# Kernel optimization log

Hardware: AMD Instinct MI355X
Metric: run time of the kernel (lower is better)

The kernel has to match this reference:

```python
import jax, jax.numpy as jnp
import numpy as np

LOG2E = 1.4426950408889634
NUM_HEADS = 12

def fake_quant_sym8(x):
    # per-tensor symmetric int8 fake-quant (QuantStub with MovingAverageMinMax,
    # symmetric, qint8 [-128,127]); dynamic scale from current amax, STE.
    scale = jnp.maximum(jnp.max(jnp.abs(x)) / 127.0, 1e-8)
    q = jnp.clip(jnp.round(x / scale), -128.0, 127.0) * scale
    return x + jax.lax.stop_gradient(q - x)

def integer_approx_softmax(x):
    # ITA-style integer-approximated softmax: exp(x) = 2^(x*log2e),
    # split into integer/fractional parts, 2^f approximated piecewise-linearly
    # as (1 + f) for f in [0,1) (hardware shift-add friendly), then normalize.
    z = x * LOG2E
    z = z - jnp.max(z, axis=-1, keepdims=True)  # z <= 0, numerically stable
    zi = jnp.floor(z)
    zf = z - zi
    p = jnp.exp2(zi) * (1.0 + zf)
    return p / jnp.sum(p, axis=-1, keepdims=True)

def setup_inputs() -> dict:
    key = jax.random.key(0)
    ks = jax.random.split(key, 5)
    B, N, E, P = 8, 1024, 768, 768
    s = 0.02  # typical init scale for linear weights
    return {
        "x":  jax.random.normal(ks[0], (B, N, E), jnp.float32),
        "Wq": jax.random.normal(ks[1], (E, P), jnp.float32) * s,
        "bq": jnp.zeros((P,), jnp.float32),
        "Wk": jax.random.normal(ks[2], (E, P), jnp.float32) * s,
        "bk": jnp.zeros((P,), jnp.float32),
        "Wv": jax.random.normal(ks[3], (E, P), jnp.float32) * s,
        "bv": jnp.zeros((P,), jnp.float32),
        "Wo": jax.random.normal(ks[4], (P, E), jnp.float32) * s,
        "bo": jnp.zeros((E,), jnp.float32),
    }

def reference(x, Wq, bq, Wk, bk, Wv, bv, Wo, bo):
    B, N, E = x.shape
    H = NUM_HEADS
    D = Wq.shape[1] // H  # head_dim = proj_dim // num_heads
    xq = fake_quant_sym8(x)
    # projections -> [B, H, N, D]
    Q = (xq @ Wq + bq).reshape(B, N, H, D).transpose(0, 2, 1, 3)
    K = (xq @ Wk + bk).reshape(B, N, H, D).transpose(0, 2, 1, 3)
    V = (xq @ Wv + bv).reshape(B, N, H, D).transpose(0, 2, 1, 3)
    # NOTE: no 1/sqrt(D) scaling -- the torch module applies none (ITA absorbs
    # scaling into the quantization parameters).
    logits = jnp.einsum('bhnd,bhmd->bhnm', Q, K)
    attn = integer_approx_softmax(logits)
    ctx = jnp.einsum('bhnm,bhmd->bhnd', attn, V)
    ctx = ctx.transpose(0, 2, 1, 3).reshape(B, N, H * D)
    return ctx @ Wo + bo
```

## Files before the change

### kernel.cpp

```cpp
#include <hip/hip_runtime.h>


typedef unsigned short u16;
typedef __attribute__((ext_vector_type(8))) short short8;
typedef __attribute__((ext_vector_type(8))) _Float16 half8;
typedef __attribute__((ext_vector_type(4))) float f32x4;

#define LOG2E_F 1.4426950408889634f

static __device__ __forceinline__ half8 s2h(short8 s) {
  union { short8 s; half8 h; } u; u.s = s; return u.h;
}
static __device__ __forceinline__ f32x4 mfma16(short8 a, short8 b, f32x4 c) {
  return __builtin_amdgcn_mfma_f32_16x16x32_f16(s2h(a), s2h(b), c, 0, 0, 0);
}
static __device__ __forceinline__ u16 f2h(float f) {
  union { _Float16 h; u16 u; } v; v.h = (_Float16)f; return v.u;
}
static __device__ __forceinline__ void gload16(const void* g, void* l) {
  __builtin_amdgcn_global_load_lds(
      (const __attribute__((address_space(1))) void*)g,
      (__attribute__((address_space(3))) void*)l, 16, 0, 0);
}

__global__ __launch_bounds__(256) void amax_part_kernel(
    const float4* __restrict__ x, float* __restrict__ part, int n4) {
  float m = 0.f;
  int i = blockIdx.x * 256 + threadIdx.x;
  const int stride = gridDim.x * 256;
  for (; i < n4; i += stride) {
    float4 v = x[i];
    m = fmaxf(m, fmaxf(fmaxf(fabsf(v.x), fabsf(v.y)),
                       fmaxf(fabsf(v.z), fabsf(v.w))));
  }
  #pragma unroll
  for (int o = 1; o < 64; o <<= 1) m = fmaxf(m, __shfl_xor(m, o));
  __shared__ float sw[4];
  if ((threadIdx.x & 63) == 0) sw[threadIdx.x >> 6] = m;
  __syncthreads();
  if (threadIdx.x == 0)
    part[blockIdx.x] = fmaxf(fmaxf(sw[0], sw[1]), fmaxf(sw[2], sw[3]));
}

__global__ __launch_bounds__(256) void amax_fin_kernel(
    const float* __restrict__ part, double* __restrict__ dsc,
    float* __restrict__ dscf) {
  const int t = threadIdx.x;
  float m = fmaxf(fmaxf(part[t], part[t + 256]),
                  fmaxf(part[t + 512], part[t + 768]));
  #pragma unroll
  for (int o = 1; o < 64; o <<= 1) m = fmaxf(m, __shfl_xor(m, o));
  __shared__ float sw[4];
  if ((t & 63) == 0) sw[t >> 6] = m;
  __syncthreads();
  if (t == 0) {
    double sd = (double)(fmaxf(fmaxf(sw[0], sw[1]), fmaxf(sw[2], sw[3]))) / 127.0;
    if (sd < 1e-8) sd = 1e-8;
    dsc[0] = sd;
    dsc[1] = 1.0 / sd;
    dscf[0] = (float)sd;
  }
}

__global__ __launch_bounds__(256) void quant_kernel(
    const float4* __restrict__ x, u16* __restrict__ xq,
    const double* __restrict__ dsc, int n4) {
  const double rinv = dsc[1];
  int i = blockIdx.x * 256 + threadIdx.x;
  const int stride = gridDim.x * 256;
  for (; i < n4; i += stride) {
    float4 v = x[i];
    ushort4 u;
    u.x = f2h((float)fmin(fmax(rint((double)v.x * rinv), -128.0), 127.0));
    u.y = f2h((float)fmin(fmax(rint((double)v.y * rinv), -128.0), 127.0));
    u.z = f2h((float)fmin(fmax(rint((double)v.z * rinv), -128.0), 127.0));
    u.w = f2h((float)fmin(fmax(rint((double)v.w * rinv), -128.0), 127.0));
    *(ushort4*)&xq[(size_t)i * 4] = u;
  }
}

__global__ __launch_bounds__(256) void prep_weights_kernel(
    const float* __restrict__ Wq, const float* __restrict__ Wk,
    const float* __restrict__ Wv, const float* __restrict__ Wo,
    const float* __restrict__ bq, const float* __restrict__ bk,
    const float* __restrict__ bv,
    u16* __restrict__ Wcat, u16* __restrict__ Wot, float* __restrict__ bcat) {
  __shared__ float t[64][65];
  const int m = blockIdx.y;
  const float* src = (m == 0) ? Wq : (m == 1) ? Wk : (m == 2) ? Wv : Wo;
  u16* dst = (m == 3) ? Wot : (Wcat + (size_t)m * 768 * 768);
  const int tile = blockIdx.x;
  const int r0 = (tile / 12) * 64, c0 = (tile - (tile / 12) * 12) * 64;
  const int i = threadIdx.x >> 6, j = threadIdx.x & 63;
  #pragma unroll
  for (int it = 0; it < 16; ++it) {
    const int row = it * 4 + i;
    t[row][j] = src[(size_t)(r0 + row) * 768 + c0 + j];
  }
  __syncthreads();
  #pragma unroll
  for (int it = 0; it < 16; ++it) {
    const int row = it * 4 + i;
    dst[(size_t)(c0 + row) * 768 + r0 + j] = f2h(t[j][row]);
  }
  if (blockIdx.x == 0 && m == 0) {
    for (int k = threadIdx.x; k < 768; k += 256) {
      bcat[k] = bq[k];
      bcat[k + 768] = bk[k];
      bcat[k + 1536] = bv[k];
    }
  }
}

template <int MODE>
__global__ __launch_bounds__(256, 4) void gemm128(
    const u16* __restrict__ A, const u16* __restrict__ Bt,
    const float* __restrict__ bias, const float* __restrict__ scale_p,
    u16* __restrict__ Oq, u16* __restrict__ Ok, u16* __restrict__ Ovt,
    float* __restrict__ Of) {
  __shared__ u16 S[4][4608];
  const int K = 768, nk = 24;
  const int tid = threadIdx.x;
  const int w = tid >> 6, l = tid & 63;
  const int l15 = l & 15, lk = l >> 4;
  const int wr = w >> 1, wc = w & 1;
  const int bid = blockIdx.x;
  const int g = bid & 7, li = bid >> 3;
  const int tn = li >> 3, tm = g * 8 + (li & 7);
  f32x4 acc[4][4] = {};
  const int rA = tid >> 2;
  const int c8 = (tid & 3) * 8;
  const u16* gA = A + (size_t)(tm * 128 + rA) * K + c8;
  const u16* gB = Bt + (size_t)(tn * 128 + rA) * K + c8;
  {
    char* lA = (char*)S[0] + w * 1024;
    char* lB = (char*)S[2] + w * 1024;
    gload16(gA, lA);
    gload16(gA + (size_t)64 * K, lA + 4096);
    gload16(gB, lB);
    gload16(gB + (size_t)64 * K, lB + 4096);
  }
  __syncthreads();
  for (int kt = 0; kt < nk; ++kt) {
    const int buf = kt & 1;
    if (kt + 1 < nk) {
      const int k0 = (kt + 1) * 32;
      char* lA = (char*)S[buf ^ 1] + w * 1024;
      char* lB = (char*)S[2 + (buf ^ 1)] + w * 1024;
      gload16(gA + k0, lA);
      gload16(gA + k0 + (size_t)64 * K, lA + 4096);
      gload16(gB + k0, lB);
      gload16(gB + k0 + (size_t)64 * K, lB + 4096);
    }
    short8 af[4], bf[4];
    #pragma unroll
    for (int mi = 0; mi < 4; ++mi)
      af[mi] = *(const short8*)&S[buf][(wr * 64 + mi * 16 + l15) * 32 + lk * 8];
    #pragma unroll
    for (int ni = 0; ni < 4; ++ni)
      bf[ni] = *(const short8*)&S[2 + buf][(wc * 64 + ni * 16 + l15) * 32 + lk * 8];
    #pragma unroll
    for (int mi = 0; mi < 4; ++mi)
      #pragma unroll
      for (int ni = 0; ni < 4; ++ni)
        acc[mi][ni] = mfma16(af[mi], bf[ni], acc[mi][ni]);
    __syncthreads();
  }

  if (MODE == 1) {
    #pragma unroll
    for (int mi = 0; mi < 4; ++mi)
      #pragma unroll
      for (int ni = 0; ni < 4; ++ni)
        #pragma unroll
        for (int j = 0; j < 4; ++j) {
          const int gm = tm * 128 + wr * 64 + mi * 16 + lk * 4 + j;
          const int c = tn * 128 + wc * 64 + ni * 16 + l15;
          Of[(size_t)gm * 768 + c] = acc[mi][ni][j] + bias[c];
        }
    return;
  }

  __syncthreads();
  const float s = *scale_p;
  const int seg = tn / 6;
  const int h = (tn - seg * 6) * 2 + wc;
  u16* esc = &S[w][0];
  #pragma unroll
  for (int mi = 0; mi < 4; ++mi) {
    #pragma unroll
    for (int ni = 0; ni < 4; ++ni) {
      #pragma unroll
      for (int j = 0; j < 4; ++j) {
        const float v = acc[mi][ni][j] * s + bias[tn * 128 + wc * 64 + ni * 16 + l15];
        const int row = mi * 16 + lk * 4 + j;
        const int col = ni * 16 + l15;
        if (seg < 2) esc[row * 72 + col] = f2h(v);
        else         esc[col * 72 + row] = f2h(v);
      }
    }
  }
  asm volatile("s_waitcnt lgkmcnt(0)" ::: "memory");
  const int n0 = tm * 128 + wr * 64;
  const int b = n0 >> 10, nn = n0 & 1023;
  u16* outp = (seg == 0) ? Oq : (seg == 1) ? Ok : Ovt;
  #pragma unroll
  for (int it = 0; it < 8; ++it) {
    const int r = it * 8 + (l >> 3);
    const int cc = (l & 7) * 8;
    short8 vv = *(const short8*)&esc[r * 72 + cc];
    size_t o;
    if (seg < 2)
      o = (((size_t)b * 12 + h) * 1024 + nn + r) * 64 + cc;
    else
      o = (((size_t)b * 12 + h) * 64 + r) * 1024 + nn + cc;
    *(short8*)&outp[o] = vv;
  }
}

__global__ __launch_bounds__(256, 3) void attn_kernel(
    const u16* __restrict__ Q, const u16* __restrict__ K,
    const u16* __restrict__ Vt, u16* __restrict__ ctx) {
  __shared__ u16 Ks[2][64 * 64];
  __shared__ u16 Vs[2][64 * 64];
  __shared__ u16 Pw[4][32 * 40];
  const int bh = blockIdx.x, qt = blockIdx.y;
  const int b = bh / 12, h = bh - b * 12;
  const int tid = threadIdx.x;
  const int w = tid >> 6, l = tid & 63;
  const int l15 = l & 15, lk = l >> 4;
  const int xr = l15 & 7;

  short8 qa[2][2];
  #pragma unroll
  for (int rf = 0; rf < 2; ++rf) {
    const size_t qoff =
        ((size_t)bh * 1024 + qt * 128 + w * 32 + rf * 16 + l15) * 64 + lk * 8;
    qa[rf][0] = *(const short8*)(Q + qoff);
    qa[rf][1] = *(const short8*)(Q + qoff + 32);
  }

  const int r8 = l >> 3;
  const int schunk = ((l & 7) ^ r8) * 8;
  const u16* Kg0 = K + ((size_t)bh * 1024 + w * 16 + r8) * 64 + schunk;
  const u16* Kg1 = Kg0 + 512;
  const u16* Vg0 = Vt + ((size_t)bh * 64 + w * 16 + r8) * 1024 + schunk;
  const u16* Vg1 = Vg0 + 8192;

  #define STAGE_K(buf, kt)                                            \
    {                                                                 \
      gload16(Kg0 + (size_t)(kt) * 4096, &Ks[buf][w * 1024]);         \
      gload16(Kg1 + (size_t)(kt) * 4096, &Ks[buf][w * 1024 + 512]);   \
    }
  #define STAGE_V(buf, kt)                                            \
    {                                                                 \
      gload16(Vg0 + (size_t)(kt) * 64, &Vs[buf][w * 1024]);           \
      gload16(Vg1 + (size_t)(kt) * 64, &Vs[buf][w * 1024 + 512]);     \
    }

  f32x4 mx[2];
  #pragma unroll
  for (int rf = 0; rf < 2; ++rf)
    #pragma unroll
    for (int j = 0; j < 4; ++j) mx[rf][j] = -3e38f;
  STAGE_K(0, 0)
  __syncthreads();
  for (int kt = 0; kt < 16; ++kt) {
    const int buf = kt & 1;
    if (kt < 15) STAGE_K(buf ^ 1, kt + 1)
    const u16* kb = Ks[buf];
    #pragma unroll
    for (int ks = 0; ks < 4; ++ks) {
      short8 k0 = *(const short8*)&kb[(ks * 16 + l15) * 64 + ((lk ^ xr) * 8)];
      short8 k1 = *(const short8*)&kb[(ks * 16 + l15) * 64 + (((lk + 4) ^ xr) * 8)];
      #pragma unroll
      for (int rf = 0; rf < 2; ++rf) {
        f32x4 sv = {0.f, 0.f, 0.f, 0.f};
        sv = mfma16(qa[rf][0], k0, sv);
        sv = mfma16(qa[rf][1], k1, sv);
        #pragma unroll
        for (int j = 0; j < 4; ++j) mx[rf][j] = fmaxf(mx[rf][j], sv[j]);
      }
    }
    __syncthreads();
  }
  f32x4 mz[2];
  #pragma unroll
  for (int rf = 0; rf < 2; ++rf) {
    #pragma unroll
    for (int o = 1; o < 16; o <<= 1) {
      #pragma unroll
      for (int j = 0; j < 4; ++j)
        mx[rf][j] = fmaxf(mx[rf][j], __shfl_xor(mx[rf][j], o));
    }
    #pragma unroll
    for (int j = 0; j < 4; ++j) mz[rf][j] = mx[rf][j] * LOG2E_F;
  }

  f32x4 sum[2] = {};
  f32x4 pv[2][4] = {};
  u16* const pw = Pw[w];
  STAGE_K(0, 0)
  STAGE_V(0, 0)
  __syncthreads();
  for (int kt = 0; kt < 16; ++kt) {
    const int buf = kt & 1;
    if (kt < 15) {
      STAGE_K(buf ^ 1, kt + 1)
      STAGE_V(buf ^ 1, kt + 1)
    }
    const u16* kb = Ks[buf];
    const u16* vb = Vs[buf];
    #pragma unroll
    for (int ko = 0; ko < 2; ++ko) {
      #pragma unroll
      for (int ks2 = 0; ks2 < 2; ++ks2) {
        const int ks = ko * 2 + ks2;
        short8 k0 = *(const short8*)&kb[(ks * 16 + l15) * 64 + ((lk ^ xr) * 8)];
        short8 k1 = *(const short8*)&kb[(ks * 16 + l15) * 64 + (((lk + 4) ^ xr) * 8)];
        #pragma unroll
        for (int rf = 0; rf < 2; ++rf) {
          f32x4 sv = {0.f, 0.f, 0.f, 0.f};
          sv = mfma16(qa[rf][0], k0, sv);
          sv = mfma16(qa[rf][1], k1, sv);
          #pragma unroll
          for (int j = 0; j < 4; ++j) {
            float z = sv[j] * LOG2E_F;
            float zz = z - mz[rf][j];
            float zi = floorf(zz);
            float p = ldexpf(1.0f + (zz - zi), (int)zi);
            sum[rf][j] += p;
            pw[(rf * 16 + lk * 4 + j) * 40 + ks2 * 16 + l15] = f2h(p);
          }
        }
      }
      asm volatile("s_waitcnt lgkmcnt(0)" ::: "memory");
      short8 pa0 = *(const short8*)&pw[l15 * 40 + lk * 8];
      short8 pa1 = *(const short8*)&pw[(16 + l15) * 40 + lk * 8];
      #pragma unroll
      for (int dt = 0; dt < 4; ++dt) {
        short8 vv = *(const short8*)&vb[(dt * 16 + l15) * 64 +
                                        (((lk + 4 * ko) ^ xr) * 8)];
        pv[0][dt] = mfma16(pa0, vv, pv[0][dt]);
        pv[1][dt] = mfma16(pa1, vv, pv[1][dt]);
      }
    }
    __syncthreads();
  }
  #undef STAGE_K
  #undef STAGE_V
  #pragma unroll
  for (int rf = 0; rf < 2; ++rf) {
    #pragma unroll
    for (int o = 1; o < 16; o <<= 1) {
      #pragma unroll
      for (int j = 0; j < 4; ++j) sum[rf][j] += __shfl_xor(sum[rf][j], o);
    }
    const int nrow = qt * 128 + w * 32 + rf * 16 + lk * 4;
    #pragma unroll
    for (int dt = 0; dt < 4; ++dt) {
      #pragma unroll
      for (int j = 0; j < 4; ++j) {
        float v = pv[rf][dt][j] / sum[rf][j];
        ctx[((size_t)b * 1024 + nrow + j) * 768 + h * 64 + dt * 16 + l15] =
            f2h(v);
      }
    }
  }
}

extern "C" void kernel_launch(void* const* d_in, const int* in_sizes, int n_in,
                              void* d_out, int out_size, void* d_ws, size_t ws_size,
                              hipStream_t stream) {
  const float* x  = (const float*)d_in[0];
  const float* Wq = (const float*)d_in[1];
  const float* bq = (const float*)d_in[2];
  const float* Wk = (const float*)d_in[3];
  const float* bk = (const float*)d_in[4];
  const float* Wv = (const float*)d_in[5];
  const float* bv = (const float*)d_in[6];
  const float* Wo = (const float*)d_in[7];
  const float* bo = (const float*)d_in[8];
  float* out = (float*)d_out;

  char* ws = (char*)d_ws;
  float* part  = (float*)ws;
  double* dsc  = (double*)(ws + 4096);
  float* dscf  = (float*)(ws + 4112);
  float* bcat  = (float*)(ws + 8192);
  size_t off = 8192 + 16384;
  const size_t WB = (size_t)768 * 768;
  const size_t XB = (size_t)8192 * 768;
  u16* xq   = (u16*)(ws + off); off += XB * 2;
  u16* Wcat = (u16*)(ws + off); off += 3 * WB * 2;
  u16* Wot  = (u16*)(ws + off); off += WB * 2;
  u16* Qb   = (u16*)(ws + off); off += XB * 2;
  u16* Kb   = (u16*)(ws + off); off += XB * 2;
  u16* Vtb  = (u16*)(ws + off); off += XB * 2;
  u16* ctx  = xq;
  (void)ws_size; (void)in_sizes; (void)n_in; (void)out_size;

  const int n4 = (8 * 1024 * 768) / 4;
  amax_part_kernel<<<1024, 256, 0, stream>>>((const float4*)x, part, n4);
  amax_fin_kernel<<<1, 256, 0, stream>>>(part, dsc, dscf);
  quant_kernel<<<2048, 256, 0, stream>>>((const float4*)x, xq, dsc, n4);
  prep_weights_kernel<<<dim3(144, 4), 256, 0, stream>>>(
      Wq, Wk, Wv, Wo, bq, bk, bv, Wcat, Wot, bcat);
  gemm128<0><<<1152, 256, 0, stream>>>(xq, Wcat, bcat, dscf,
                                       Qb, Kb, Vtb, nullptr);
  attn_kernel<<<dim3(96, 8), 256, 0, stream>>>(Qb, Kb, Vtb, ctx);
  gemm128<1><<<384, 256, 0, stream>>>(ctx, Wot, bo, nullptr,
                                      nullptr, nullptr, nullptr, out);
}
```

Measured before the change: 144.4 us.

## Compute ITA exp via float bit trick and deepen K prefetch in max pass

Replaces the floor/ldexp evaluation of the piecewise-linear 2^z with a single FMA plus an int conversion reinterpreted as a float. This exploits the fact that (1+f)*2^i is exactly the IEEE bit pattern linear in z, after clamping z at -126. The max pass is also restructured to use one shared LDS buffer with four K stages, prefetching two tiles ahead per barrier and halving the barrier count. The bit trick truncates rather than rounds, so it may differ slightly in the last bit, and the clamp changes how tiny values underflow.

```diff
diff --git a/kernel.cpp b/kernel.cpp
--- a/kernel.cpp
+++ b/kernel.cpp
@@ -16,6 +16,13 @@
 }
 static __device__ __forceinline__ u16 f2h(float f) {
   union { _Float16 h; u16 u; } v; v.h = (_Float16)f; return v.u;
+}
+static __device__ __forceinline__ float ita_p(float zz) {
+  zz = fmaxf(zz, -126.0f);
+  float t = fmaf(zz, 8388608.0f, 1065353216.0f);
+  union { int i; float f; } c;
+  c.i = (int)t;
+  return c.f;
 }
 static __device__ __forceinline__ void gload16(const void* g, void* l) {
   __builtin_amdgcn_global_load_lds(
@@ -221,9 +228,9 @@
 __global__ __launch_bounds__(256, 3) void attn_kernel(
     const u16* __restrict__ Q, const u16* __restrict__ K,
     const u16* __restrict__ Vt, u16* __restrict__ ctx) {
-  __shared__ u16 Ks[2][64 * 64];
-  __shared__ u16 Vs[2][64 * 64];
-  __shared__ u16 Pw[4][32 * 40];
+  __shared__ u16 lds[4 * 4096 + 4 * 1280];
+  u16* const ldsK = lds;
+  u16* const ldsV = lds + 8192;
   const int bh = blockIdx.x, qt = blockIdx.y;
   const int b = bh / 12, h = bh - b * 12;
   const int tid = threadIdx.x;
@@ -247,15 +254,17 @@
   const u16* Vg0 = Vt + ((size_t)bh * 64 + w * 16 + r8) * 1024 + schunk;
   const u16* Vg1 = Vg0 + 8192;
 
-  #define STAGE_K(buf, kt)                                            \
-    {                                                                 \
-      gload16(Kg0 + (size_t)(kt) * 4096, &Ks[buf][w * 1024]);         \
-      gload16(Kg1 + (size_t)(kt) * 4096, &Ks[buf][w * 1024 + 512]);   \
-    }
-  #define STAGE_V(buf, kt)                                            \
-    {                                                                 \
-      gload16(Vg0 + (size_t)(kt) * 64, &Vs[buf][w * 1024]);           \
-      gload16(Vg1 + (size_t)(kt) * 64, &Vs[buf][w * 1024 + 512]);     \
+  #define STAGE_KA(buf, kt)                                                 \
+    {                                                                       \
+      gload16(Kg0 + (size_t)(kt) * 4096, &ldsK[(buf) * 4096 + w * 1024]);   \
+      gload16(Kg1 + (size_t)(kt) * 4096,                                    \
+              &ldsK[(buf) * 4096 + w * 1024 + 512]);                        \
+    }
+  #define STAGE_V(buf, kt)                                                  \
+    {                                                                       \
+      gload16(Vg0 + (size_t)(kt) * 64, &ldsV[(buf) * 4096 + w * 1024]);     \
+      gload16(Vg1 + (size_t)(kt) * 64,                                      \
+              &ldsV[(buf) * 4096 + w * 1024 + 512]);                        \
     }
 
   f32x4 mx[2];
@@ -263,28 +272,34 @@
   for (int rf = 0; rf < 2; ++rf)
     #pragma unroll
     for (int j = 0; j < 4; ++j) mx[rf][j] = -3e38f;
-  STAGE_K(0, 0)
-  __syncthreads();
-  for (int kt = 0; kt < 16; ++kt) {
-    const int buf = kt & 1;
-    if (kt < 15) STAGE_K(buf ^ 1, kt + 1)
-    const u16* kb = Ks[buf];
-    #pragma unroll
-    for (int ks = 0; ks < 4; ++ks) {
-      short8 k0 = *(const short8*)&kb[(ks * 16 + l15) * 64 + ((lk ^ xr) * 8)];
-      short8 k1 = *(const short8*)&kb[(ks * 16 + l15) * 64 + (((lk + 4) ^ xr) * 8)];
-      #pragma unroll
-      for (int rf = 0; rf < 2; ++rf) {
-        f32x4 sv = {0.f, 0.f, 0.f, 0.f};
-        sv = mfma16(qa[rf][0], k0, sv);
-        sv = mfma16(qa[rf][1], k1, sv);
+  STAGE_KA(0, 0)
+  STAGE_KA(1, 1)
+  __syncthreads();
+  for (int st = 0; st < 8; ++st) {
+    if (st < 7) {
+      STAGE_KA((2 * st + 2) & 3, 2 * st + 2)
+      STAGE_KA((2 * st + 3) & 3, 2 * st + 3)
+    }
+    #pragma unroll
+    for (int hf = 0; hf < 2; ++hf) {
+      const u16* kb = &ldsK[((2 * st + hf) & 3) * 4096];
+      #pragma unroll
+      for (int ks = 0; ks < 4; ++ks) {
+        short8 k0 = *(const short8*)&kb[(ks * 16 + l15) * 64 + ((lk ^ xr) * 8)];
+        short8 k1 = *(const short8*)&kb[(ks * 16 + l15) * 64 + (((lk + 4) ^ xr) * 8)];
         #pragma unroll
-        for (int j = 0; j < 4; ++j) mx[rf][j] = fmaxf(mx[rf][j], sv[j]);
+        for (int rf = 0; rf < 2; ++rf) {
+          f32x4 sv = {0.f, 0.f, 0.f, 0.f};
+          sv = mfma16(qa[rf][0], k0, sv);
+          sv = mfma16(qa[rf][1], k1, sv);
+          #pragma unroll
+          for (int j = 0; j < 4; ++j) mx[rf][j] = fmaxf(mx[rf][j], sv[j]);
+        }
       }
     }
     __syncthreads();
   }
-  f32x4 mz[2];
+  f32x4 negmz[2];
   #pragma unroll
   for (int rf = 0; rf < 2; ++rf) {
     #pragma unroll
@@ -294,23 +309,23 @@
         mx[rf][j] = fmaxf(mx[rf][j], __shfl_xor(mx[rf][j], o));
     }
     #pragma unroll
-    for (int j = 0; j < 4; ++j) mz[rf][j] = mx[rf][j] * LOG2E_F;
+    for (int j = 0; j < 4; ++j) negmz[rf][j] = -(mx[rf][j] * LOG2E_F);
   }
 
   f32x4 sum[2] = {};
   f32x4 pv[2][4] = {};
-  u16* const pw = Pw[w];
-  STAGE_K(0, 0)
+  u16* const pw = &lds[16384 + w * 1280];
+  STAGE_KA(0, 0)
   STAGE_V(0, 0)
   __syncthreads();
   for (int kt = 0; kt < 16; ++kt) {
     const int buf = kt & 1;
     if (kt < 15) {
-      STAGE_K(buf ^ 1, kt + 1)
+      STAGE_KA(buf ^ 1, kt + 1)
       STAGE_V(buf ^ 1, kt + 1)
     }
-    const u16* kb = Ks[buf];
-    const u16* vb = Vs[buf];
+    const u16* kb = &ldsK[buf * 4096];
+    const u16* vb = &ldsV[buf * 4096];
     #pragma unroll
     for (int ko = 0; ko < 2; ++ko) {
       #pragma unroll
@@ -325,10 +340,7 @@
           sv = mfma16(qa[rf][1], k1, sv);
           #pragma unroll
           for (int j = 0; j < 4; ++j) {
-            float z = sv[j] * LOG2E_F;
-            float zz = z - mz[rf][j];
-            float zi = floorf(zz);
-            float p = ldexpf(1.0f + (zz - zi), (int)zi);
+            float p = ita_p(fmaf(sv[j], LOG2E_F, negmz[rf][j]));
             sum[rf][j] += p;
             pw[(rf * 16 + lk * 4 + j) * 40 + ks2 * 16 + l15] = f2h(p);
           }
@@ -347,7 +359,7 @@
     }
     __syncthreads();
   }
-  #undef STAGE_K
+  #undef STAGE_KA
   #undef STAGE_V
   #pragma unroll
   for (int rf = 0; rf < 2; ++rf) {
```

Result: slower. 149.5 us (+3.5%).
